# Kernel optimization log

Measured on AMD Instinct MI355X. Metric: run time of the kernel, lower is better.

Reference implementation:

```python
import jax, jax.numpy as jnp
import numpy as np

N, M = 120000, 32
VX, VY = 0.16, 0.16
X_OFF = VX / 2 + 0.0          # vx/2 + pc_range[0]
Y_OFF = VY / 2 + (-39.68)     # vy/2 + pc_range[1]
BN_EPS = 1e-3


def setup_inputs() -> dict:
    key = jax.random.key(0)
    k1, k2, k3, k4, k5 = jax.random.split(key, 5)
    features = jax.random.normal(k1, (N, M, 4), dtype=jnp.float32)
    num_points = jax.random.randint(k2, (N,), 1, M + 1)              # >=1 point per pillar
    cy = jax.random.randint(k3, (N, 1), 0, 496)
    cx = jax.random.randint(k4, (N, 1), 0, 432)
    zeros = jnp.zeros((N, 2), dtype=jnp.int32)
    coors = jnp.concatenate([zeros, cy, cx], axis=1)                 # (N,4): [b, z, y, x]
    W = jax.random.normal(k5, (63, 9), dtype=jnp.float32) * 0.1      # Linear(9->63), no bias
    gamma = jnp.ones((63,), jnp.float32)
    beta = jnp.zeros((63,), jnp.float32)
    running_mean = jnp.zeros((63,), jnp.float32)
    running_var = jnp.ones((63,), jnp.float32)
    return {"features": features, "num_points": num_points, "coors": coors,
            "W": W, "gamma": gamma, "beta": beta,
            "running_mean": running_mean, "running_var": running_var}


def reference(features, num_points, coors, W, gamma, beta, running_mean, running_var):
    dt = features.dtype
    npf = num_points.astype(dt)[:, None, None]                        # (N,1,1)
    # distance to pillar centroid (xyz mean over points)
    voxels_mean = features[:, :, :3].sum(axis=1, keepdims=True) / npf
    centroid_dist = features[:, :, :3] - voxels_mean                  # (N,M,3)
    # offset from pillar base center (detached in the original)
    fxy = jax.lax.stop_gradient(features[:, :, :2])
    cx = fxy[:, :, 0] - (coors[:, 3].astype(dt)[:, None] * VX + X_OFF)
    cy = fxy[:, :, 1] - (coors[:, 2].astype(dt)[:, None] * VY + Y_OFF)
    base_center = jnp.stack([cx, cy], axis=-1)                        # (N,M,2)
    feats = jnp.concatenate([features, centroid_dist, base_center], axis=-1)  # (N,M,9)
    # zero out padded points
    mask = (jnp.arange(feats.shape[1])[None, :] < num_points[:, None]).astype(dt)[:, :, None]
    feats = feats * mask
    # PFNLayer (last layer, mode='max'): linear -> BN (eval stats) -> relu -> max over points
    x = jnp.einsum('nmc,uc->nmu', feats, W)                           # (N,M,63)
    inv = gamma / jnp.sqrt(running_var + BN_EPS)
    x = x * inv + (beta - running_mean * inv)
    x = jax.nn.relu(x)
    x_max = x.max(axis=1)                                             # (N,63)
    return jnp.concatenate([x_max, num_points.astype(dt)[:, None]], axis=-1)  # (N,64)
```

## Files before the change

### kernel.cpp

```cpp
#include <hip/hip_runtime.h>

typedef unsigned int u32;
typedef unsigned short u16;
typedef __attribute__((ext_vector_type(8))) short bf16x8;
typedef __attribute__((ext_vector_type(16))) float f32x16;
typedef __attribute__((ext_vector_type(4))) u32 u32x4;


#define XOFF (0.08f)
#define YOFF (0.08f - 39.68f)

__device__ __forceinline__ u32 f2bf_bits(float f) {
    union { float f; u32 u; } v; v.f = f;
    u32 u = v.u;
    u += 0x7fffu + ((u >> 16) & 1u);
    return u >> 16;
}
__device__ __forceinline__ u32 pk2(float lo, float hi) {
    return f2bf_bits(lo) | (f2bf_bits(hi) << 16);
}
__device__ __forceinline__ short bf1(float f) { return (short)f2bf_bits(f); }

__device__ __forceinline__ float vmax16(const f32x16 v) {
    float a = fmaxf(fmaxf(v[0], v[1]), fmaxf(v[2], v[3]));
    float b = fmaxf(fmaxf(v[4], v[5]), fmaxf(v[6], v[7]));
    float c = fmaxf(fmaxf(v[8], v[9]), fmaxf(v[10], v[11]));
    float d = fmaxf(fmaxf(v[12], v[13]), fmaxf(v[14], v[15]));
    return fmaxf(fmaxf(a, b), fmaxf(c, d));
}

__global__ __launch_bounds__(256, 4)
void pfn_mfma(const float* __restrict__ features,
              const int* __restrict__ num_points,
              const int* __restrict__ coors,
              const float* __restrict__ W,
              const float* __restrict__ gamma,
              const float* __restrict__ beta,
              const float* __restrict__ rmean,
              const float* __restrict__ rvar,
              float* __restrict__ out,
              int n_total)
{
    __shared__ __align__(16) u16 lds[4][64 * 24];

    const int lane = threadIdx.x & 63;
    const int wid  = threadIdx.x >> 6;
    const int half = lane >> 5;
    const int m    = lane & 31;
    const int waves_total = gridDim.x * 4;
    const int gwave = blockIdx.x * 4 + wid;

    const int c0 = m, c1 = 32 + m;
    const float inv0   = gamma[c0] / sqrtf(rvar[c0] + 1e-3f);
    const float shift0 = beta[c0] - rmean[c0] * inv0;
    float inv1 = 0.0f, shift1 = 0.0f;
    if (c1 < 63) {
        inv1   = gamma[c1] / sqrtf(rvar[c1] + 1e-3f);
        shift1 = beta[c1] - rmean[c1] * inv1;
    }
    const float shift_me = half ? shift1 : shift0;

    bf16x8 b0, b1;
#pragma unroll
    for (int j = 0; j < 8; ++j) {
        const int k = half * 8 + j;
        const float w0v = (k < 9) ? W[c0 * 9 + k] * inv0 : 0.0f;
        const float w1v = (k < 9 && c1 < 63) ? W[c1 * 9 + k] * inv1 : 0.0f;
        b0[j] = bf1(w0v);
        b1[j] = bf1(w1v);
    }

    const float4* featv = reinterpret_cast<const float4*>(features);
    const int pairs_per_sweep = waves_total;
    const int iters = (n_total + 2 * waves_total - 1) / (2 * waves_total);

    for (int it = 0; it < iters; ++it) {
        const int pair = gwave + it * pairs_per_sweep;
        const int nA   = pair * 2;
        const int n_h  = nA + half;
        const bool act = (n_h < n_total);

        const int npts = act ? num_points[n_h] : 1;
        float cxo = 0.f, cyo = 0.f;
        float4 q = make_float4(0.f, 0.f, 0.f, 0.f);
        if (act) {
            cxo = (float)coors[n_h * 4 + 3] * 0.16f + XOFF;
            cyo = (float)coors[n_h * 4 + 2] * 0.16f + YOFF;
            q = featv[(size_t)n_h * 32 + m];
        }

        float sx = q.x, sy = q.y, sz = q.z;
#pragma unroll
        for (int d = 1; d < 32; d <<= 1) {
            sx += __shfl_xor(sx, d, 32);
            sy += __shfl_xor(sy, d, 32);
            sz += __shfl_xor(sz, d, 32);
        }
        const float rnp = 1.0f / (float)npts;
        const float mx = sx * rnp, my = sy * rnp, mz = sz * rnp;

        const bool valid = (m < npts);
        float f0 = 0.f, f1 = 0.f, f2 = 0.f, f3 = 0.f, f4 = 0.f,
              f5 = 0.f, f6 = 0.f, f7 = 0.f, f8 = 0.f;
        if (valid) {
            f0 = q.x; f1 = q.y; f2 = q.z; f3 = q.w;
            f4 = q.x - mx; f5 = q.y - my; f6 = q.z - mz;
            f7 = q.x - cxo; f8 = q.y - cyo;
        }

        u16* row = &lds[wid][lane * 24];
        u32x4 lodw; lodw[0] = pk2(f0, f1); lodw[1] = pk2(f2, f3);
        lodw[2] = pk2(f4, f5); lodw[3] = pk2(f6, f7);
        u32x4 hidw; hidw[0] = pk2(f8, 0.f); hidw[1] = 0; hidw[2] = 0; hidw[3] = 0;
        reinterpret_cast<u32x4*>(row)[0] = lodw;
        reinterpret_cast<u32x4*>(row)[1] = hidw;
        __syncthreads();

        const bf16x8 aA = *reinterpret_cast<const bf16x8*>(&lds[wid][m * 24 + half * 8]);
        const bf16x8 aB = *reinterpret_cast<const bf16x8*>(&lds[wid][(32 + m) * 24 + half * 8]);

        f32x16 cA0 = {}, cA1 = {}, cB0 = {}, cB1 = {};
        cA0 = __builtin_amdgcn_mfma_f32_32x32x16_bf16(aA, b0, cA0, 0, 0, 0);
        cA1 = __builtin_amdgcn_mfma_f32_32x32x16_bf16(aA, b1, cA1, 0, 0, 0);
        cB0 = __builtin_amdgcn_mfma_f32_32x32x16_bf16(aB, b0, cB0, 0, 0, 0);
        cB1 = __builtin_amdgcn_mfma_f32_32x32x16_bf16(aB, b1, cB1, 0, 0, 0);

        float tA0 = vmax16(cA0), tA1 = vmax16(cA1);
        float tB0 = vmax16(cB0), tB1 = vmax16(cB1);
        tA0 = fmaxf(tA0, __shfl_xor(tA0, 32));
        tA1 = fmaxf(tA1, __shfl_xor(tA1, 32));
        tB0 = fmaxf(tB0, __shfl_xor(tB0, 32));
        tB1 = fmaxf(tB1, __shfl_xor(tB1, 32));

        float vA = fmaxf((half ? tA1 : tA0) + shift_me, 0.0f);
        float vB = fmaxf((half ? tB1 : tB0) + shift_me, 0.0f);

        const float npf = (float)npts;
        const float npA = __shfl(npf, 0);
        const float npB = __shfl(npf, 32);
        if (lane == 63) { vA = npA; vB = npB; }

        if (nA < n_total)     out[(size_t)nA * 64 + lane] = vA;
        if (nA + 1 < n_total) out[(size_t)(nA + 1) * 64 + lane] = vB;

        __syncthreads();
    }
}

extern "C" void kernel_launch(void* const* d_in, const int* in_sizes, int n_in,
                              void* d_out, int out_size, void* d_ws, size_t ws_size,
                              hipStream_t stream) {
    const float* features   = (const float*)d_in[0];
    const int*   num_points = (const int*)d_in[1];
    const int*   coors      = (const int*)d_in[2];
    const float* W          = (const float*)d_in[3];
    const float* gamma      = (const float*)d_in[4];
    const float* beta       = (const float*)d_in[5];
    const float* rmean      = (const float*)d_in[6];
    const float* rvar       = (const float*)d_in[7];
    float* out              = (float*)d_out;

    const int n_total = in_sizes[1];

    const int blocks = 1024;
    pfn_mfma<<<blocks, 256, 0, stream>>>(features, num_points, coors, W,
                                         gamma, beta, rmean, rvar, out, n_total);
}
```

Before: 135.1 us.

## Prefetch next pillar pair and replace LDS transpose with cross-lane shuffles

Loads for the next iteration's pillar pair (features, num_points, coords) are issued before the current pair is processed, so global memory latency overlaps compute. The LDS staging buffer and both block-wide __syncthreads are removed, and the MFMA A operands are built with __shfl_xor across the two half-waves. The packed bf16 conversion now uses the HIP intrinsic. This costs extra registers for the prefetched values and adds shuffle traffic, but removes block-level barriers.

```diff
diff --git a/kernel.cpp b/kernel.cpp
--- a/kernel.cpp
+++ b/kernel.cpp
@@ -1,4 +1,5 @@
 #include <hip/hip_runtime.h>
+#include <hip/hip_bf16.h>
 
 typedef unsigned int u32;
 typedef unsigned short u16;
@@ -16,10 +17,13 @@
     u += 0x7fffu + ((u >> 16) & 1u);
     return u >> 16;
 }
+__device__ __forceinline__ short bf1(float f) { return (short)f2bf_bits(f); }
+
 __device__ __forceinline__ u32 pk2(float lo, float hi) {
-    return f2bf_bits(lo) | (f2bf_bits(hi) << 16);
+    __hip_bfloat162 h = __float22bfloat162_rn(make_float2(lo, hi));
+    union { __hip_bfloat162 h; u32 u; } v; v.h = h;
+    return v.u;
 }
-__device__ __forceinline__ short bf1(float f) { return (short)f2bf_bits(f); }
 
 __device__ __forceinline__ float vmax16(const f32x16 v) {
     float a = fmaxf(fmaxf(v[0], v[1]), fmaxf(v[2], v[3]));
@@ -41,8 +45,6 @@
               float* __restrict__ out,
               int n_total)
 {
-    __shared__ __align__(16) u16 lds[4][64 * 24];
-
     const int lane = threadIdx.x & 63;
     const int wid  = threadIdx.x >> 6;
     const int half = lane >> 5;
@@ -64,29 +66,40 @@
 #pragma unroll
     for (int j = 0; j < 8; ++j) {
         const int k = half * 8 + j;
-        const float w0v = (k < 9) ? W[c0 * 9 + k] * inv0 : 0.0f;
-        const float w1v = (k < 9 && c1 < 63) ? W[c1 * 9 + k] * inv1 : 0.0f;
-        b0[j] = bf1(w0v);
-        b1[j] = bf1(w1v);
+        b0[j] = bf1((k < 9) ? W[c0 * 9 + k] * inv0 : 0.0f);
+        b1[j] = bf1((k < 9 && c1 < 63) ? W[c1 * 9 + k] * inv1 : 0.0f);
     }
 
     const float4* featv = reinterpret_cast<const float4*>(features);
-    const int pairs_per_sweep = waves_total;
     const int iters = (n_total + 2 * waves_total - 1) / (2 * waves_total);
 
-    for (int it = 0; it < iters; ++it) {
-        const int pair = gwave + it * pairs_per_sweep;
-        const int nA   = pair * 2;
-        const int n_h  = nA + half;
-        const bool act = (n_h < n_total);
-
-        const int npts = act ? num_points[n_h] : 1;
-        float cxo = 0.f, cyo = 0.f;
-        float4 q = make_float4(0.f, 0.f, 0.f, 0.f);
-        if (act) {
+    float4 q = make_float4(0.f, 0.f, 0.f, 0.f);
+    int   npts = 1;
+    float cxo = 0.f, cyo = 0.f;
+    {
+        const int n_h = gwave * 2 + half;
+        if (n_h < n_total) {
+            npts = num_points[n_h];
             cxo = (float)coors[n_h * 4 + 3] * 0.16f + XOFF;
             cyo = (float)coors[n_h * 4 + 2] * 0.16f + YOFF;
             q = featv[(size_t)n_h * 32 + m];
+        }
+    }
+
+    for (int it = 0; it < iters; ++it) {
+        const int nA = (gwave + it * waves_total) * 2;
+
+        float4 qn = make_float4(0.f, 0.f, 0.f, 0.f);
+        int   npn = 1;
+        float cxn = 0.f, cyn = 0.f;
+        if (it + 1 < iters) {
+            const int n_h = (gwave + (it + 1) * waves_total) * 2 + half;
+            if (n_h < n_total) {
+                npn = num_points[n_h];
+                cxn = (float)coors[n_h * 4 + 3] * 0.16f + XOFF;
+                cyn = (float)coors[n_h * 4 + 2] * 0.16f + YOFF;
+                qn = featv[(size_t)n_h * 32 + m];
+            }
         }
 
         float sx = q.x, sy = q.y, sz = q.z;
@@ -99,25 +112,26 @@
         const float rnp = 1.0f / (float)npts;
         const float mx = sx * rnp, my = sy * rnp, mz = sz * rnp;
 
-        const bool valid = (m < npts);
-        float f0 = 0.f, f1 = 0.f, f2 = 0.f, f3 = 0.f, f4 = 0.f,
-              f5 = 0.f, f6 = 0.f, f7 = 0.f, f8 = 0.f;
-        if (valid) {
-            f0 = q.x; f1 = q.y; f2 = q.z; f3 = q.w;
-            f4 = q.x - mx; f5 = q.y - my; f6 = q.z - mz;
-            f7 = q.x - cxo; f8 = q.y - cyo;
-        }
+        u32 p0 = pk2(q.x, q.y);
+        u32 p1 = pk2(q.z, q.w);
+        u32 p2 = pk2(q.x - mx, q.y - my);
+        u32 p3 = pk2(q.z - mz, q.x - cxo);
+        u32 p4 = pk2(q.y - cyo, 0.0f);
+        if (m >= npts) { p0 = 0; p1 = 0; p2 = 0; p3 = 0; p4 = 0; }
 
-        u16* row = &lds[wid][lane * 24];
-        u32x4 lodw; lodw[0] = pk2(f0, f1); lodw[1] = pk2(f2, f3);
-        lodw[2] = pk2(f4, f5); lodw[3] = pk2(f6, f7);
-        u32x4 hidw; hidw[0] = pk2(f8, 0.f); hidw[1] = 0; hidw[2] = 0; hidw[3] = 0;
-        reinterpret_cast<u32x4*>(row)[0] = lodw;
-        reinterpret_cast<u32x4*>(row)[1] = hidw;
-        __syncthreads();
+        const u32 x0 = __shfl_xor(p0, 32);
+        const u32 x1 = __shfl_xor(p1, 32);
+        const u32 x2 = __shfl_xor(p2, 32);
+        const u32 x3 = __shfl_xor(p3, 32);
+        const u32 x4 = __shfl_xor(p4, 32);
 
-        const bf16x8 aA = *reinterpret_cast<const bf16x8*>(&lds[wid][m * 24 + half * 8]);
-        const bf16x8 aB = *reinterpret_cast<const bf16x8*>(&lds[wid][(32 + m) * 24 + half * 8]);
+        u32x4 adw, bdw;
+        adw[0] = half ? x4 : p0;  adw[1] = half ? 0u : p1;
+        adw[2] = half ? 0u : p2;  adw[3] = half ? 0u : p3;
+        bdw[0] = half ? p4 : x0;  bdw[1] = half ? 0u : x1;
+        bdw[2] = half ? 0u : x2;  bdw[3] = half ? 0u : x3;
+        const bf16x8 aA = __builtin_bit_cast(bf16x8, adw);
+        const bf16x8 aB = __builtin_bit_cast(bf16x8, bdw);
 
         f32x16 cA0 = {}, cA1 = {}, cB0 = {}, cB1 = {};
         cA0 = __builtin_amdgcn_mfma_f32_32x32x16_bf16(aA, b0, cA0, 0, 0, 0);
@@ -143,7 +157,7 @@
         if (nA < n_total)     out[(size_t)nA * 64 + lane] = vA;
         if (nA + 1 < n_total) out[(size_t)(nA + 1) * 64 + lane] = vB;
 
-        __syncthreads();
+        q = qn; npts = npn; cxo = cxn; cyo = cyn;
     }
 }
 
```

Result: no change. 132.8 us (-1.7%).
